# Kernel optimization log

Measured on AMD Instinct MI355X. Metric: run time of the kernel, lower is better.

Reference implementation:

```python
import jax, jax.numpy as jnp
import numpy as np

# ---- helpers ----

def _conv2d(x, w, pad):
    # x (N,Cin,H,W), w (Cout,Cin,kh,kw), stride 1, zero padding `pad`
    return jax.lax.conv_general_dilated(
        x, w, (1, 1), ((pad, pad), (pad, pad)),
        dimension_numbers=('NCHW', 'OIHW', 'NCHW'))


def _deform_conv3x3(x, offset, w):
    # DCNv1 (torchvision deform_conv2d semantics), kernel 3, pad 1, dilation 1, no bias.
    # x (P,C,H,W), offset (P,18,H,W) ordered [tap, (dy,dx)], w (O,C,3,3)
    P, C, H, W = x.shape
    off = offset.reshape(P, 9, 2, H, W)
    ky, kx = jnp.meshgrid(jnp.arange(3), jnp.arange(3), indexing='ij')
    ky = ky.reshape(9)
    kx = kx.reshape(9)
    base_y = (jnp.arange(H)[None, :, None] + (ky - 1)[:, None, None]).astype(x.dtype)  # (9,H,1)
    base_x = (jnp.arange(W)[None, None, :] + (kx - 1)[:, None, None]).astype(x.dtype)  # (9,1,W)
    py = base_y[None] + off[:, :, 0]  # (P,9,H,W) sampling rows
    px = base_x[None] + off[:, :, 1]  # (P,9,H,W) sampling cols
    y0 = jnp.floor(py)
    x0 = jnp.floor(px)
    ty = py - y0
    tx = px - x0
    xf = x.reshape(P, C, H * W)

    def gather(yi, xi):
        valid = ((yi >= 0) & (yi < H) & (xi >= 0) & (xi < W)).astype(x.dtype)
        idx = (jnp.clip(yi, 0, H - 1) * W + jnp.clip(xi, 0, W - 1)).astype(jnp.int32)
        v = jnp.take_along_axis(xf, idx.reshape(P, 1, 9 * H * W), axis=2)
        return v.reshape(P, C, 9, H, W) * valid[:, None]

    y0i = y0.astype(jnp.int32)
    x0i = x0.astype(jnp.int32)
    v00 = gather(y0i, x0i)
    v01 = gather(y0i, x0i + 1)
    v10 = gather(y0i + 1, x0i)
    v11 = gather(y0i + 1, x0i + 1)
    ty_ = ty[:, None]
    tx_ = tx[:, None]
    samp = (v00 * (1 - ty_) * (1 - tx_) + v01 * (1 - ty_) * tx_ +
            v10 * ty_ * (1 - tx_) + v11 * ty_ * tx_)  # (P,C,9,H,W)
    return jnp.einsum('pckhw,ock->pohw', samp, w.reshape(w.shape[0], C, 9))


def _apply_dynamic(q, filt):
    # DynamicWeights.forward body: unfold 3x3 (pad 1) + per-position bmm + relu.
    P, C, H, W = q.shape
    qp = jnp.pad(q, ((0, 0), (0, 0), (1, 1), (1, 1)))
    # im2col patches, tap order (dy outer, dx inner) matching nn.Unfold
    patches = jnp.stack([qp[:, :, dy:dy + H, dx:dx + W]
                         for dy in range(3) for dx in range(3)], axis=2)  # (P,C,9,H,W)
    f = filt.reshape(-1, 9)  # faithful flat row-major reshape, (P*H*W, 9)
    xp = patches.transpose(0, 3, 4, 1, 2).reshape(P * H * W, C, 9)
    out = jnp.einsum('pck,pk->pc', xp, f)
    out = out.reshape(P, H, W, C).transpose(0, 3, 1, 2)
    return jax.nn.relu(out)


def _forward(support_feat, query_feat, support_targets, w_off, w_def):
    b, ns, C, H, W = support_feat.shape
    nq = query_feat.shape[1]
    K = support_targets.shape[2]
    # class prototypes: bmm(Y^T, feats) / counts
    Yt = support_targets.transpose(0, 2, 1)  # (b,K,ns)
    feat = support_feat.reshape(b, ns, C * H * W)
    proto = jnp.einsum('bkn,bnf->bkf', Yt, feat) / jnp.sum(Yt, axis=2, keepdims=True)
    proto = proto.reshape(b, K, C, H, W)
    n1, n2 = K, nq
    ftrain = jnp.broadcast_to(proto[:, None], (b, n2, n1, C, H, W))
    ftest = jnp.broadcast_to(query_feat[:, :, None], (b, n2, n1, C, H, W))
    P = b * n1 * n2
    ftr = ftrain.reshape(P, C, H, W)
    fte = ftest.reshape(P, C, H, W)
    # DynamicWeights_: offset conv (cat[query,support]) -> deform conv -> sigmoid
    offset = _conv2d(jnp.concatenate([fte, ftr], axis=1), w_off, 2)  # (P,18,H,W)
    filt = jax.nn.sigmoid(_deform_conv3x3(ftr, offset, w_def))       # (P,9,H,W)
    # ODEBlock: torchdiffeq method='rk4' on t=[0,1] -> one 3/8-rule step, dt=1.
    # filter component has zero derivative, so it stays constant.
    g = lambda q: _apply_dynamic(q, filt)
    k1 = g(fte)
    k2 = g(fte + k1 / 3.0)
    k3 = g(fte + (k2 - k1 / 3.0))
    k4 = g(fte + (k1 - k2 + k3))
    scores = fte + (k1 + 3.0 * (k2 + k3) + k4) / 8.0  # (P,C,H,W)
    # conv_weight: L2-normalize prototypes over channel dim, spatial mean
    norm = jnp.maximum(jnp.linalg.norm(ftrain, axis=3, keepdims=True), 1e-12)
    cw = (ftrain / norm).reshape(P, C, H, W).mean(axis=(2, 3))  # (P,C)
    # grouped 1x1 conv with padding=1 -> per-pair channel dot on zero-padded scores
    sp = jnp.pad(scores, ((0, 0), (0, 0), (1, 1), (1, 1)))
    cls = jnp.einsum('pchw,pc->phw', sp, cw)
    cls = cls.reshape(b * n2, n1, H + 2, W + 2)
    # eval path: get_test_score = spatial mean
    return cls.mean(axis=(2, 3))  # (b*n2, n1)


def setup_inputs() -> dict:
    key = jax.random.key(0)
    ks = jax.random.split(key, 5)
    b, n_way, n_shot, n_query = 2, 5, 5, 16
    C, H, W = 640, 5, 5
    ns = n_way * n_shot
    support_feat = jax.random.normal(ks[0], (b, ns, C, H, W), jnp.float32)
    query_feat = jax.random.normal(ks[1], (b, n_query, C, H, W), jnp.float32)
    labels = jnp.arange(ns) % n_way
    support_targets = jnp.tile(jax.nn.one_hot(labels, n_way, dtype=jnp.float32)[None], (b, 1, 1))
    qlabels = jax.random.randint(ks[2], (b, n_query), 0, n_way)
    query_targets = jax.nn.one_hot(qlabels, n_way, dtype=jnp.float32)
    w_off = jax.random.normal(ks[3], (18, 2 * C, 5, 5), jnp.float32) * 0.01
    w_def = jax.random.normal(ks[4], (9, C, 3, 3), jnp.float32) * 0.02
    return {'support_feat': support_feat, 'query_feat': query_feat,
            'support_targets': support_targets, 'query_targets': query_targets,
            'w_off': w_off, 'w_def': w_def}


def reference(support_feat, query_feat, support_targets, query_targets, w_off, w_def):
    # query_targets is only used in training mode (global classifier); eval path ignores it.
    return _forward(support_feat, query_feat, support_targets, w_off, w_def)
```

## Files before the change

### kernel.cpp

```cpp
#include <hip/hip_runtime.h>
#include <math.h>

#define BB 2
#define NS 25
#define NQ 16
#define KW 5
#define C  640
#define HW 25
#define C2 1280
#define P  160

typedef unsigned short ushort_t;
typedef unsigned int uint_t;
typedef __attribute__((ext_vector_type(8))) short short8;
typedef __attribute__((ext_vector_type(4))) short short4v;
typedef __attribute__((ext_vector_type(16))) float f32x16;

#define WS_PROTO   0
#define WS_WDH     160000
#define WS_WDL     252160
#define WS_CW      344320
#define WS_PART    350720
#define WS_WMFH    351520
#define WS_OFFP    863520
#define WS_FILTP   2015520

static __device__ inline ushort_t f2bf(float x) {
    uint_t u = __float_as_uint(x);
    uint_t r = (u + 0x7FFFu + ((u >> 16) & 1u)) >> 16;
    return (ushort_t)r;
}
static __device__ inline float bf2f(ushort_t b) {
    return __uint_as_float(((uint_t)b) << 16);
}

#define PB_PROTO 1563
#define PB_WMF   500
#define PB_WDF   90
__global__ void k_prep(const float* __restrict__ sf, const float* __restrict__ st,
                       const float* __restrict__ w_off, const float* __restrict__ w_def,
                       float* __restrict__ proto, ushort_t* __restrict__ wh,
                       ushort_t* __restrict__ wdh, ushort_t* __restrict__ wdl) {
    int b = blockIdx.x;
    int tid = threadIdx.x;
    if (b < PB_PROTO) {
        int idx = b * 256 + tid;
        if (idx >= BB * KW * C * HW) return;
        int hw = idx % HW; int r = idx / HW;
        int c = r % C; r /= C;
        int k = r % KW; int bi = r / KW;
        float num = 0.f, den = 0.f;
        for (int n = 0; n < NS; ++n) {
            float w = st[(bi * NS + n) * KW + k];
            num += w * sf[((bi * NS + n) * C + c) * HW + hw];
            den += w;
        }
        proto[idx] = num / den;
    } else if (b < PB_PROTO + PB_WMF) {
        int idx = (b - PB_PROTO) * 256 + tid;
        int lane = idx & 63;
        int r = idx >> 6;
        int c16 = r % 5; r /= 5;
        int t = r % 25;
        int kc = r / 25;
        int o = lane & 31;
        int cb = kc * 80 + c16 * 16 + ((lane >> 5) << 3);
        union { short8 v; ushort_t u[8]; } hs;
        #pragma unroll
        for (int j = 0; j < 8; ++j) {
            float w = (o < 18) ? w_off[((size_t)o * C2 + cb + j) * 25 + t] : 0.f;
            hs.u[j] = f2bf(w);
        }
        *(short8*)(wh + (size_t)idx * 8) = hs.v;
    } else {
        int idx = (b - PB_PROTO - PB_WMF) * 256 + tid;
        if (idx >= 8 * 45 * 64) return;
        int lane = idx & 63;
        int r = idx >> 6;
        int s = r % 45;
        int kc = r / 45;
        int o = lane & 31;
        int kbase = s * 16 + ((lane >> 5) << 3);
        union { short8 v; ushort_t u[8]; } hs, ls;
        #pragma unroll
        for (int j = 0; j < 8; ++j) {
            int k_lin = kbase + j;
            int c_local = k_lin / 9, kk = k_lin - 9 * c_local;
            float w = (o < 9) ? w_def[((size_t)o * C + kc * 80 + c_local) * 9 + kk] : 0.f;
            ushort_t h = f2bf(w);
            hs.u[j] = h;
            ls.u[j] = f2bf(w - bf2f(h));
        }
        *(short8*)(wdh + (size_t)idx * 8) = hs.v;
        *(short8*)(wdl + (size_t)idx * 8) = ls.v;
    }
}

__launch_bounds__(256)
__attribute__((amdgpu_waves_per_eu(4, 4)))
__global__ void k_off(const float* __restrict__ qf, const float* __restrict__ proto,
                      const ushort_t* __restrict__ wh, float* __restrict__ offp,
                      float* __restrict__ cw) {
    __shared__ __align__(16) float scr[4096];
    int tid = threadIdx.x;
    if (blockIdx.x >= 1280) {
        float* nr = scr;
        float* inv = scr + 256;
        int blk = blockIdx.x - 1280;
        const float* base = proto + (size_t)blk * C * HW;
        if (tid < 250) {
            int hw = tid / 10, sl = tid % 10;
            float s = 0.f;
            for (int c = sl; c < C; c += 10) { float v = base[c * HW + hw]; s += v * v; }
            nr[tid] = s;
        }
        __syncthreads();
        if (tid < 25) {
            float s = 0.f;
            #pragma unroll
            for (int j = 0; j < 10; ++j) s += nr[tid * 10 + j];
            inv[tid] = 1.f / fmaxf(sqrtf(s), 1e-12f);
        }
        __syncthreads();
        for (int c = tid; c < C; c += 256) {
            float s = 0.f;
            #pragma unroll
            for (int hw = 0; hw < HW; ++hw) s += base[c * HW + hw] * inv[hw];
            cw[(size_t)blk * C + c] = s * (1.f / 25.f);
        }
        return;
    }
    ushort_t* B0 = (ushort_t*)scr;
    ushort_t* B1 = (ushort_t*)scr + 2392;
    int g = blockIdx.x >> 4, kc = blockIdx.x & 15;
    int cbase = kc * 80;
    int lane = tid & 63, wv = tid >> 6;

    for (int i = tid; i < 2392; i += 256) ((uint_t*)B0)[i] = 0u;
    __syncthreads();
    for (int i = tid; i < 4000; i += 256) {
        int j = i / 2000, e = i % 2000;
        int cc = e / 25, pp = e % 25;
        int p = g * 2 + j;
        int bi = p / (NQ * KW); int rem = p % (NQ * KW);
        int q = rem / KW; int k = rem % KW;
        const float* src = (cbase < C)
            ? qf + ((bi * NQ + q) * C + cbase) * HW
            : proto + ((bi * KW + k) * C + (cbase - C)) * HW;
        (j ? B1 : B0)[(1 + pp) * 92 + cc] = f2bf(src[e]);
    }
    __syncthreads();

    int hw = lane & 31;
    int by = hw / 5, bx = hw % 5;
    int laneCh = (lane >> 5) * 8;
    const ushort_t* whp = wh + (size_t)kc * 64000 + lane * 8;

    f32x16 acc0, acc1;
    #pragma unroll
    for (int r = 0; r < 16; ++r) { acc0[r] = 0.f; acc1[r] = 0.f; }

    union U8 { short8 v8; short4v v4[2]; };

    for (int t = wv; t < 25; t += 4) {
        int ty = t / 5, tx = t % 5;
        int ry = by + ty - 2, rx = bx + tx - 2;
        bool valid = (ry >= 0 && ry < 5 && rx >= 0 && rx < 5);
        int row = valid ? (1 + ry * 5 + rx) : 0;
        int base0 = row * 92 + laneCh;
        const ushort_t* ahp = whp + (size_t)t * 2560;
        #pragma unroll
        for (int c16 = 0; c16 < 5; ++c16) {
            short8 a_h = *(const short8*)(ahp + c16 * 512);
            U8 b0, b1;
            b0.v4[0] = *(const short4v*)(B0 + base0 + c16 * 16);
            b0.v4[1] = *(const short4v*)(B0 + base0 + c16 * 16 + 4);
            b1.v4[0] = *(const short4v*)(B1 + base0 + c16 * 16);
            b1.v4[1] = *(const short4v*)(B1 + base0 + c16 * 16 + 4);
            acc0 = __builtin_amdgcn_mfma_f32_32x32x16_bf16(a_h, b0.v8, acc0, 0, 0, 0);
            acc1 = __builtin_amdgcn_mfma_f32_32x32x16_bf16(a_h, b1.v8, acc1, 0, 0, 0);
        }
    }

    #define EMIT_PAIR(J, ACC)                                                   \
    {                                                                           \
        __syncthreads();                                                        \
        _Pragma("unroll")                                                       \
        for (int r = 0; r < 16; ++r) scr[r * 256 + tid] = ACC[r];               \
        __syncthreads();                                                        \
        int p = g * 2 + (J);                                                    \
        float* dst = offp + ((size_t)p * 16 + kc) * 450;                        \
        for (int i = tid; i < 450; i += 256) {                                  \
            int o = i / 25, hw2 = i % 25;                                       \
            int r = (o & 3) | ((o >> 3) << 2);                                  \
            int ln = hw2 + ((o >> 2) & 1) * 32;                                 \
            float s = scr[r * 256 + ln] + scr[r * 256 + 64 + ln]                \
                    + scr[r * 256 + 128 + ln] + scr[r * 256 + 192 + ln];        \
            dst[o * 25 + hw2] = s;                                              \
        }                                                                       \
    }
    EMIT_PAIR(0, acc0)
    EMIT_PAIR(1, acc1)
    #undef EMIT_PAIR
}

__launch_bounds__(256)
__global__ void k_def(const float* __restrict__ proto, const float* __restrict__ offp,
                      const ushort_t* __restrict__ wdh, const ushort_t* __restrict__ wdl,
                      float* __restrict__ filtp) {
    __shared__ __align__(16) float plds[2000];
    __shared__ __align__(16) ushort_t samp[25 * 728];
    int p = blockIdx.x, kc = blockIdx.y;
    int bi = p / (NQ * KW); int rem = p % (NQ * KW);
    int k = rem % KW;
    const float* ftr = proto + ((bi * KW + k) * C + kc * 80) * HW;
    int tid = threadIdx.x, lane = tid & 63, wv = tid >> 6;

    for (int i = tid; i < 2000; i += 256) plds[i] = ftr[i];
    __syncthreads();

    if (tid < 225) {
        int kk = tid / 25, hw = tid % 25;
        float offY = 0.f, offX = 0.f;
        for (int kcc = 0; kcc < 16; ++kcc) {
            const float* ob = offp + ((size_t)p * 16 + kcc) * 450;
            offY += ob[(kk * 2 + 0) * 25 + hw];
            offX += ob[(kk * 2 + 1) * 25 + hw];
        }
        int h = hw / 5, w = hw % 5, ky = kk / 3, kx = kk % 3;
        float py = (float)(h + ky - 1) + offY;
        float px = (float)(w + kx - 1) + offX;
        float y0f = floorf(py), x0f = floorf(px);
        float ty = py - y0f, tx = px - x0f;
        int y0 = (int)y0f, x0 = (int)x0f;
        int y1 = y0 + 1, x1 = x0 + 1;
        bool vy0 = (y0 >= 0 && y0 < 5), vy1 = (y1 >= 0 && y1 < 5);
        bool vx0 = (x0 >= 0 && x0 < 5), vx1 = (x1 >= 0 && x1 < 5);
        int cy0 = min(max(y0, 0), 4), cy1 = min(max(y1, 0), 4);
        int cx0 = min(max(x0, 0), 4), cx1 = min(max(x1, 0), 4);
        int i0 = cy0 * 5 + cx0, i1 = cy0 * 5 + cx1;
        int i2 = cy1 * 5 + cx0, i3 = cy1 * 5 + cx1;
        float wb0 = (vy0 && vx0) ? (1.f - ty) * (1.f - tx) : 0.f;
        float wb1 = (vy0 && vx1) ? (1.f - ty) * tx : 0.f;
        float wb2 = (vy1 && vx0) ? ty * (1.f - tx) : 0.f;
        float wb3 = (vy1 && vx1) ? ty * tx : 0.f;
        for (int c = 0; c < 80; ++c) {
            const float* base = &plds[c * 25];
            float s = wb0 * base[i0] + wb1 * base[i1] + wb2 * base[i2] + wb3 * base[i3];
            samp[hw * 728 + c * 9 + kk] = f2bf(s);
        }
    }
    __syncthreads();

    int hwr = (lane & 31) < 25 ? (lane & 31) : 0;
    int k8 = (lane >> 5) * 8;
    const ushort_t* ahp = wdh + ((size_t)kc * 45 * 64 + lane) * 8;
    const ushort_t* alp = wdl + ((size_t)kc * 45 * 64 + lane) * 8;

    f32x16 acc;
    #pragma unroll
    for (int r = 0; r < 16; ++r) acc[r] = 0.f;

    for (int s = wv; s < 45; s += 4) {
        short8 b = *(const short8*)(samp + hwr * 728 + s * 16 + k8);
        short8 a_l = *(const short8*)(alp + (size_t)s * 512);
        short8 a_h = *(const short8*)(ahp + (size_t)s * 512);
        acc = __builtin_amdgcn_mfma_f32_32x32x16_bf16(a_l, b, acc, 0, 0, 0);
        acc = __builtin_amdgcn_mfma_f32_32x32x16_bf16(a_h, b, acc, 0, 0, 0);
    }

    __syncthreads();
    float* scr = (float*)samp;
    #pragma unroll
    for (int r = 0; r < 16; ++r) scr[r * 256 + tid] = acc[r];
    __syncthreads();

    float* dst = filtp + ((size_t)p * 8 + kc) * 225;
    for (int i = tid; i < 225; i += 256) {
        int o = i / 25, hw2 = i % 25;
        int r = (o & 3) | ((o >> 3) << 2);
        int ln = hw2 + ((o >> 2) & 1) * 32;
        float s = scr[r * 256 + ln] + scr[r * 256 + 64 + ln]
                + scr[r * 256 + 128 + ln] + scr[r * 256 + 192 + ln];
        dst[o * 25 + hw2] = s;
    }
}

#define GSTEP(QA, KA)                                                       \
    {                                                                       \
        _Pragma("unroll")                                                   \
        for (int hw_ = 0; hw_ < 25; ++hw_) {                                \
            const int h_ = hw_ / 5, w_ = hw_ % 5;                           \
            float s_ = 0.f;                                                 \
            _Pragma("unroll")                                               \
            for (int kp_ = 0; kp_ < 9; ++kp_) {                             \
                const int y_ = h_ + kp_ / 3 - 1, x_ = w_ + kp_ % 3 - 1;     \
                if (y_ >= 0 && y_ < 5 && x_ >= 0 && x_ < 5)                 \
                    s_ = fmaf(QA[y_ * 5 + x_], fl[hw_ * 9 + kp_], s_);      \
            }                                                               \
            KA[hw_] = fmaxf(s_, 0.f);                                       \
        }                                                                   \
    }

__launch_bounds__(128)
__global__ void k_rk(const float* __restrict__ qf, const float* __restrict__ filtp,
                     const float* __restrict__ cw, float* __restrict__ part) {
    __shared__ float fl[225];
    __shared__ float qlds[3200];
    __shared__ float wsum[2];
    int bid = blockIdx.x;
    int p = bid / 5, ch = bid % 5;
    int bi = p / (NQ * KW); int rem = p % (NQ * KW);
    int q = rem / KW; int k = rem % KW;
    int tid = threadIdx.x;
    int c = ch * 128 + tid;
    for (int i = tid; i < 225; i += 128) {
        float s = 0.f;
        #pragma unroll
        for (int cs = 0; cs < 8; ++cs) s += filtp[((size_t)p * 8 + cs) * 225 + i];
        fl[i] = 1.f / (1.f + expf(-s));
    }
    const float* qbase = qf + ((bi * NQ + q) * C + ch * 128) * HW;
    for (int i = tid; i < 3200; i += 128) qlds[i] = qbase[i];
    __syncthreads();

    float F[25], K1[25], K2[25], K3[25], Q[25];
    #pragma unroll
    for (int i = 0; i < 25; ++i) F[i] = qlds[tid * 25 + i];

    GSTEP(F, K1);
    #pragma unroll
    for (int i = 0; i < 25; ++i) Q[i] = F[i] + K1[i] * (1.f / 3.f);
    GSTEP(Q, K2);
    #pragma unroll
    for (int i = 0; i < 25; ++i) Q[i] = F[i] + K2[i] - K1[i] * (1.f / 3.f);
    GSTEP(Q, K3);
    #pragma unroll
    for (int i = 0; i < 25; ++i) {
        Q[i] = F[i] + K1[i] - K2[i] + K3[i];
        K1[i] += 3.f * (K2[i] + K3[i]);
    }
    GSTEP(Q, K3);

    float S = 0.f;
    #pragma unroll
    for (int i = 0; i < 25; ++i) S += F[i] + (K1[i] + K3[i]) * 0.125f;

    float val = cw[(bi * KW + k) * C + c] * S;
    #pragma unroll
    for (int off = 32; off > 0; off >>= 1) val += __shfl_down(val, off, 64);
    if ((tid & 63) == 0) wsum[tid >> 6] = val;
    __syncthreads();
    if (tid == 0) part[p * 5 + ch] = wsum[0] + wsum[1];
}

__global__ void k_fin(const float* __restrict__ part, float* __restrict__ out) {
    int i = blockIdx.x * 256 + threadIdx.x;
    if (i < P) {
        float s = 0.f;
        #pragma unroll
        for (int ch = 0; ch < 5; ++ch) s += part[i * 5 + ch];
        out[i] = s * (1.f / 49.f);
    }
}

extern "C" void kernel_launch(void* const* d_in, const int* in_sizes, int n_in,
                              void* d_out, int out_size, void* d_ws, size_t ws_size,
                              hipStream_t stream) {
    const float* sf    = (const float*)d_in[0];
    const float* qf    = (const float*)d_in[1];
    const float* st    = (const float*)d_in[2];
    const float* w_off = (const float*)d_in[4];
    const float* w_def = (const float*)d_in[5];
    float* out = (float*)d_out;
    float* ws  = (float*)d_ws;
    ushort_t* wmfh = (ushort_t*)(ws + WS_WMFH);
    ushort_t* wdh  = (ushort_t*)(ws + WS_WDH);
    ushort_t* wdl  = (ushort_t*)(ws + WS_WDL);

    k_prep<<<PB_PROTO + PB_WMF + PB_WDF, 256, 0, stream>>>(
        sf, st, w_off, w_def, ws + WS_PROTO, wmfh, wdh, wdl);
    k_off<<<1290, 256, 0, stream>>>(qf, ws + WS_PROTO, wmfh, ws + WS_OFFP, ws + WS_CW);
    k_def<<<dim3(P, 8), 256, 0, stream>>>(ws + WS_PROTO, ws + WS_OFFP, wdh, wdl, ws + WS_FILTP);
    k_rk<<<P * 5, 128, 0, stream>>>(qf, ws + WS_FILTP, ws + WS_CW, ws + WS_PART);
    k_fin<<<1, 256, 0, stream>>>(ws + WS_PART, out);
}
```

Before: 86.44 us.

## Process four positions per offset-conv block and fold final reduction into k_rk

The offset-conv MFMA kernel now handles four (query,class) pairs per block instead of two. Each bf16 weight fragment loaded from global memory is reused across four MFMAs, and the grid is halved. The separate k_fin launch is removed: k_rk blocks use an atomic counter per pair so the last finishing block sums the partials and writes the output. A counter-zeroing block is added to k_prep. The cost is more accumulator registers and LDS in k_off, fewer blocks to spread across CUs, and atomic/fence overhead in k_rk.

```diff
diff --git a/kernel.cpp b/kernel.cpp
--- a/kernel.cpp
+++ b/kernel.cpp
@@ -21,9 +21,10 @@
 #define WS_WDL     252160
 #define WS_CW      344320
 #define WS_PART    350720
-#define WS_WMFH    351520
-#define WS_OFFP    863520
-#define WS_FILTP   2015520
+#define WS_CNT     351520
+#define WS_WMFH    351680
+#define WS_OFFP    863680
+#define WS_FILTP   2015680
 
 static __device__ inline ushort_t f2bf(float x) {
     uint_t u = __float_as_uint(x);
@@ -40,7 +41,8 @@
 __global__ void k_prep(const float* __restrict__ sf, const float* __restrict__ st,
                        const float* __restrict__ w_off, const float* __restrict__ w_def,
                        float* __restrict__ proto, ushort_t* __restrict__ wh,
-                       ushort_t* __restrict__ wdh, ushort_t* __restrict__ wdl) {
+                       ushort_t* __restrict__ wdh, ushort_t* __restrict__ wdl,
+                       int* __restrict__ cnt) {
     int b = blockIdx.x;
     int tid = threadIdx.x;
     if (b < PB_PROTO) {
@@ -72,7 +74,7 @@
             hs.u[j] = f2bf(w);
         }
         *(short8*)(wh + (size_t)idx * 8) = hs.v;
-    } else {
+    } else if (b < PB_PROTO + PB_WMF + PB_WDF) {
         int idx = (b - PB_PROTO - PB_WMF) * 256 + tid;
         if (idx >= 8 * 45 * 64) return;
         int lane = idx & 63;
@@ -93,6 +95,8 @@
         }
         *(short8*)(wdh + (size_t)idx * 8) = hs.v;
         *(short8*)(wdl + (size_t)idx * 8) = ls.v;
+    } else {
+        if (tid < P) cnt[tid] = 0;
     }
 }
 
@@ -101,12 +105,12 @@
 __global__ void k_off(const float* __restrict__ qf, const float* __restrict__ proto,
                       const ushort_t* __restrict__ wh, float* __restrict__ offp,
                       float* __restrict__ cw) {
-    __shared__ __align__(16) float scr[4096];
+    __shared__ __align__(16) float scr[4784];
     int tid = threadIdx.x;
-    if (blockIdx.x >= 1280) {
+    if (blockIdx.x >= 640) {
         float* nr = scr;
         float* inv = scr + 256;
-        int blk = blockIdx.x - 1280;
+        int blk = blockIdx.x - 640;
         const float* base = proto + (size_t)blk * C * HW;
         if (tid < 250) {
             int hw = tid / 10, sl = tid % 10;
@@ -130,24 +134,23 @@
         }
         return;
     }
-    ushort_t* B0 = (ushort_t*)scr;
-    ushort_t* B1 = (ushort_t*)scr + 2392;
+    ushort_t* B = (ushort_t*)scr;
     int g = blockIdx.x >> 4, kc = blockIdx.x & 15;
     int cbase = kc * 80;
     int lane = tid & 63, wv = tid >> 6;
 
-    for (int i = tid; i < 2392; i += 256) ((uint_t*)B0)[i] = 0u;
-    __syncthreads();
-    for (int i = tid; i < 4000; i += 256) {
+    for (int i = tid; i < 4784; i += 256) ((uint_t*)B)[i] = 0u;
+    __syncthreads();
+    for (int i = tid; i < 8000; i += 256) {
         int j = i / 2000, e = i % 2000;
         int cc = e / 25, pp = e % 25;
-        int p = g * 2 + j;
+        int p = g * 4 + j;
         int bi = p / (NQ * KW); int rem = p % (NQ * KW);
         int q = rem / KW; int k = rem % KW;
         const float* src = (cbase < C)
             ? qf + ((bi * NQ + q) * C + cbase) * HW
             : proto + ((bi * KW + k) * C + (cbase - C)) * HW;
-        (j ? B1 : B0)[(1 + pp) * 92 + cc] = f2bf(src[e]);
+        B[j * 2392 + (1 + pp) * 92 + cc] = f2bf(src[e]);
     }
     __syncthreads();
 
@@ -156,9 +159,9 @@
     int laneCh = (lane >> 5) * 8;
     const ushort_t* whp = wh + (size_t)kc * 64000 + lane * 8;
 
-    f32x16 acc0, acc1;
-    #pragma unroll
-    for (int r = 0; r < 16; ++r) { acc0[r] = 0.f; acc1[r] = 0.f; }
+    f32x16 acc0, acc1, acc2, acc3;
+    #pragma unroll
+    for (int r = 0; r < 16; ++r) { acc0[r] = 0.f; acc1[r] = 0.f; acc2[r] = 0.f; acc3[r] = 0.f; }
 
     union U8 { short8 v8; short4v v4[2]; };
 
@@ -172,13 +175,20 @@
         #pragma unroll
         for (int c16 = 0; c16 < 5; ++c16) {
             short8 a_h = *(const short8*)(ahp + c16 * 512);
-            U8 b0, b1;
-            b0.v4[0] = *(const short4v*)(B0 + base0 + c16 * 16);
-            b0.v4[1] = *(const short4v*)(B0 + base0 + c16 * 16 + 4);
-            b1.v4[0] = *(const short4v*)(B1 + base0 + c16 * 16);
-            b1.v4[1] = *(const short4v*)(B1 + base0 + c16 * 16 + 4);
+            int boff = base0 + c16 * 16;
+            U8 b0, b1, b2, b3;
+            b0.v4[0] = *(const short4v*)(B + 0 * 2392 + boff);
+            b0.v4[1] = *(const short4v*)(B + 0 * 2392 + boff + 4);
+            b1.v4[0] = *(const short4v*)(B + 1 * 2392 + boff);
+            b1.v4[1] = *(const short4v*)(B + 1 * 2392 + boff + 4);
+            b2.v4[0] = *(const short4v*)(B + 2 * 2392 + boff);
+            b2.v4[1] = *(const short4v*)(B + 2 * 2392 + boff + 4);
+            b3.v4[0] = *(const short4v*)(B + 3 * 2392 + boff);
+            b3.v4[1] = *(const short4v*)(B + 3 * 2392 + boff + 4);
             acc0 = __builtin_amdgcn_mfma_f32_32x32x16_bf16(a_h, b0.v8, acc0, 0, 0, 0);
             acc1 = __builtin_amdgcn_mfma_f32_32x32x16_bf16(a_h, b1.v8, acc1, 0, 0, 0);
+            acc2 = __builtin_amdgcn_mfma_f32_32x32x16_bf16(a_h, b2.v8, acc2, 0, 0, 0);
+            acc3 = __builtin_amdgcn_mfma_f32_32x32x16_bf16(a_h, b3.v8, acc3, 0, 0, 0);
         }
     }
 
@@ -188,7 +198,7 @@
         _Pragma("unroll")                                                       \
         for (int r = 0; r < 16; ++r) scr[r * 256 + tid] = ACC[r];               \
         __syncthreads();                                                        \
-        int p = g * 2 + (J);                                                    \
+        int p = g * 4 + (J);                                                    \
         float* dst = offp + ((size_t)p * 16 + kc) * 450;                        \
         for (int i = tid; i < 450; i += 256) {                                  \
             int o = i / 25, hw2 = i % 25;                                       \
@@ -201,6 +211,8 @@
     }
     EMIT_PAIR(0, acc0)
     EMIT_PAIR(1, acc1)
+    EMIT_PAIR(2, acc2)
+    EMIT_PAIR(3, acc3)
     #undef EMIT_PAIR
 }
 
@@ -304,7 +316,8 @@
 
 __launch_bounds__(128)
 __global__ void k_rk(const float* __restrict__ qf, const float* __restrict__ filtp,
-                     const float* __restrict__ cw, float* __restrict__ part) {
+                     const float* __restrict__ cw, float* __restrict__ part,
+                     int* __restrict__ cnt, float* __restrict__ out) {
     __shared__ float fl[225];
     __shared__ float qlds[3200];
     __shared__ float wsum[2];
@@ -351,16 +364,18 @@
     for (int off = 32; off > 0; off >>= 1) val += __shfl_down(val, off, 64);
     if ((tid & 63) == 0) wsum[tid >> 6] = val;
     __syncthreads();
-    if (tid == 0) part[p * 5 + ch] = wsum[0] + wsum[1];
-}
-
-__global__ void k_fin(const float* __restrict__ part, float* __restrict__ out) {
-    int i = blockIdx.x * 256 + threadIdx.x;
-    if (i < P) {
-        float s = 0.f;
-        #pragma unroll
-        for (int ch = 0; ch < 5; ++ch) s += part[i * 5 + ch];
-        out[i] = s * (1.f / 49.f);
+    if (tid == 0) {
+        part[p * 5 + ch] = wsum[0] + wsum[1];
+        __threadfence();
+        int old = atomicAdd(&cnt[p], 1);
+        if (old == 4) {
+            __threadfence();
+            const volatile float* pp = part + p * 5;
+            float s = 0.f;
+            #pragma unroll
+            for (int c2 = 0; c2 < 5; ++c2) s += pp[c2];
+            out[p] = s * (1.f / 49.f);
+        }
     }
 }
 
@@ -377,11 +392,11 @@
     ushort_t* wmfh = (ushort_t*)(ws + WS_WMFH);
     ushort_t* wdh  = (ushort_t*)(ws + WS_WDH);
     ushort_t* wdl  = (ushort_t*)(ws + WS_WDL);
-
-    k_prep<<<PB_PROTO + PB_WMF + PB_WDF, 256, 0, stream>>>(
-        sf, st, w_off, w_def, ws + WS_PROTO, wmfh, wdh, wdl);
-    k_off<<<1290, 256, 0, stream>>>(qf, ws + WS_PROTO, wmfh, ws + WS_OFFP, ws + WS_CW);
+    int* cnt = (int*)(ws + WS_CNT);
+
+    k_prep<<<PB_PROTO + PB_WMF + PB_WDF + 1, 256, 0, stream>>>(
+        sf, st, w_off, w_def, ws + WS_PROTO, wmfh, wdh, wdl, cnt);
+    k_off<<<650, 256, 0, stream>>>(qf, ws + WS_PROTO, wmfh, ws + WS_OFFP, ws + WS_CW);
     k_def<<<dim3(P, 8), 256, 0, stream>>>(ws + WS_PROTO, ws + WS_OFFP, wdh, wdl, ws + WS_FILTP);
-    k_rk<<<P * 5, 128, 0, stream>>>(qf, ws + WS_FILTP, ws + WS_CW, ws + WS_PART);
-    k_fin<<<1, 256, 0, stream>>>(ws + WS_PART, out);
-}
+    k_rk<<<P * 5, 128, 0, stream>>>(qf, ws + WS_FILTP, ws + WS_CW, ws + WS_PART, cnt, out);
+}
```

Result: slower. 99.20 us (+14.8%).
